# Optimization experiments

Hardware: AMD Instinct MI355X
Metric: run time of the kernel (lower is better)

Reference implementation:

```python
import jax, jax.numpy as jnp
import numpy as np

HIDDEN = 450
DEPTH = 6
ATOM_FDIM = 35          # len(ELEM_LIST)+6+5+1
BOND_FDIM = 5
MAX_NB = 15
N_ATOMS = 20000
N_BONDS = 40000
N_MESS = 16000          # tree messages (row 0 is the zero padding slot)
N_MOLS = 1000


def _linear_init(key, out_dim, in_dim):
    s = 1.0 / np.sqrt(in_dim)
    return jax.random.uniform(key, (out_dim, in_dim), jnp.float32, -s, s)


def setup_inputs() -> dict:
    key = jax.random.key(0)
    ks = jax.random.split(key, 9)
    total_msg = N_MESS + N_BONDS
    fatoms = jax.random.normal(ks[0], (N_ATOMS, ATOM_FDIM), jnp.float32)
    fbonds = jax.random.normal(ks[1], (N_BONDS, ATOM_FDIM + BOND_FDIM), jnp.float32)
    agraph = jax.random.randint(ks[2], (N_ATOMS, MAX_NB), 0, total_msg, jnp.int32)
    bgraph = jax.random.randint(ks[3], (N_BONDS, MAX_NB), 0, total_msg, jnp.int32)
    tree_message = jax.random.normal(ks[4], (N_MESS, HIDDEN), jnp.float32)
    tree_message = tree_message.at[0].set(0.0)  # index 0 = padding message
    # uniform scope: N_MOLS molecules of N_ATOMS//N_MOLS atoms each
    mol_ids = jnp.repeat(jnp.arange(N_MOLS, dtype=jnp.int32), N_ATOMS // N_MOLS)
    W_i = _linear_init(ks[5], HIDDEN, ATOM_FDIM + BOND_FDIM)
    W_h = _linear_init(ks[6], HIDDEN, HIDDEN)
    W_o = _linear_init(ks[7], HIDDEN, ATOM_FDIM + HIDDEN)
    s = 1.0 / np.sqrt(ATOM_FDIM + HIDDEN)
    b_o = jax.random.uniform(ks[8], (HIDDEN,), jnp.float32, -s, s)
    return {"fatoms": fatoms, "fbonds": fbonds, "agraph": agraph, "bgraph": bgraph,
            "mol_ids": mol_ids, "n_mols": N_MOLS, "tree_message": tree_message,
            "W_i": W_i, "W_h": W_h, "W_o": W_o, "b_o": b_o}


def reference(fatoms, fbonds, agraph, bgraph, mol_ids, n_mols, tree_message,
              W_i, W_h, W_o, b_o):
    binput = fbonds @ W_i.T                       # [B, H]
    graph_message = jax.nn.relu(binput)
    for _ in range(DEPTH - 1):                    # static depth loop
        message = jnp.concatenate([tree_message, graph_message], axis=0)  # [M+B, H]
        nei_message = message[bgraph].sum(axis=1)  # gather [B, MAX_NB, H] -> [B, H]
        graph_message = jax.nn.relu(binput + nei_message @ W_h.T)
    message = jnp.concatenate([tree_message, graph_message], axis=0)
    nei_message = message[agraph].sum(axis=1)      # [A, H]
    ainput = jnp.concatenate([fatoms, nei_message], axis=1)  # [A, ATOM_FDIM+H]
    atom_hiddens = jax.nn.relu(ainput @ W_o.T + b_o)          # [A, H]
    # mean over each molecule's atoms (scope)
    sums = jax.ops.segment_sum(atom_hiddens, mol_ids, num_segments=n_mols)
    counts = jax.ops.segment_sum(jnp.ones((atom_hiddens.shape[0], 1), atom_hiddens.dtype),
                                 mol_ids, num_segments=n_mols)
    return sums / counts
```

## Files before the change

kernel.cpp:

```cpp
#include <hip/hip_runtime.h>

#define HIDDEN 450
#define MAX_NB 15
#define N_ATOMS 20000
#define N_BONDS 40000
#define N_MESS  16000
#define N_MOLS  1000
#define KPAD    512
#define MSTRIDE 456

typedef unsigned int uint;
typedef unsigned short ushort;
typedef __bf16 bf16x8 __attribute__((ext_vector_type(8)));
typedef float  f32x4  __attribute__((ext_vector_type(4)));

__device__ __forceinline__ ushort f2bf(float f) {
    uint u = __builtin_bit_cast(uint, f);
    u += 0x7fffu + ((u >> 16) & 1u);
    return (ushort)(u >> 16);
}
__device__ __forceinline__ float bfhi(uint w) {
    return __builtin_bit_cast(float, w & 0xffff0000u);
}
__device__ __forceinline__ float bflo(uint w) {
    return __builtin_bit_cast(float, w << 16);
}

#define GLOADLDS16(g, l) __builtin_amdgcn_global_load_lds( \
    (const __attribute__((address_space(1))) void*)(g),    \
    (__attribute__((address_space(3))) void*)(l), 16, 0, 0)


__global__ __launch_bounds__(256) void pack_tree(const float* __restrict__ tree,
                                                 ushort* __restrict__ tbuf) {
    const int r = blockIdx.x, t = threadIdx.x;
    if (t < 228) {
        uint p = 0;
        if (t < 225) {
            const float2 v = *(const float2*)&tree[(size_t)r * HIDDEN + 2 * t];
            p = (uint)f2bf(v.x) | ((uint)f2bf(v.y) << 16);
        }
        ((uint*)(tbuf + (size_t)r * MSTRIDE))[t] = p;
    }
}

__global__ __launch_bounds__(256) void pack_bonds(const float* __restrict__ fbonds,
                                                  ushort* __restrict__ Abuf) {
    const int r = blockIdx.x * 4 + (threadIdx.x >> 6);
    const int t = threadIdx.x & 63;
    if (r >= N_BONDS) return;
    ushort* row = Abuf + (size_t)r * KPAD;
    if (t < 40) row[t] = f2bf(fbonds[(size_t)r * 40 + t]);
    else        row[t] = 0;
    if (t < 16) row[496 + t] = 0;
}

__global__ __launch_bounds__(256) void pack_atoms(const float* __restrict__ fatoms,
                                                  ushort* __restrict__ Aout) {
    const int r = blockIdx.x * 4 + (threadIdx.x >> 6);
    const int t = threadIdx.x & 63;
    if (r >= N_ATOMS) return;
    ushort* row = Aout + (size_t)r * KPAD;
    if (t < 40) row[t] = (t < 35) ? f2bf(fatoms[(size_t)r * 35 + t]) : (ushort)0;
    if (t < 16) row[496 + t] = 0;
}

__global__ __launch_bounds__(256) void pack_w(const float* __restrict__ W_i,
                                              const float* __restrict__ W_h,
                                              const float* __restrict__ W_o,
                                              ushort* __restrict__ Wcat,
                                              ushort* __restrict__ Wocat) {
    const int n = blockIdx.x;
    for (int c = threadIdx.x; c < KPAD; c += 256) {
        float v = 0.0f, vo = 0.0f;
        if (n < HIDDEN) {
            if (c < 40)       v = W_i[(size_t)n * 40 + c];
            else if (c < 490) v = W_h[(size_t)n * HIDDEN + (c - 40)];
            if (c < 35)       vo = W_o[(size_t)n * 485 + c];
            else if (c >= 40 && c < 490) vo = W_o[(size_t)n * 485 + 35 + (c - 40)];
        }
        Wcat [(size_t)n * KPAD + c] = f2bf(v);
        Wocat[(size_t)n * KPAD + c] = f2bf(vo);
    }
}

__global__ __launch_bounds__(256) void gather_sum(const int* __restrict__ g,
                                                  const ushort* __restrict__ tbuf,
                                                  const ushort* __restrict__ gmsg,
                                                  ushort* __restrict__ dst, int nrows) {
    const int r = blockIdx.x * 4 + (threadIdx.x >> 6);
    const int lane = threadIdx.x & 63;
    if (r >= nrows) return;
    const int* gr = g + (size_t)r * MAX_NB;
    int idx[MAX_NB];
#pragma unroll
    for (int j = 0; j < MAX_NB; ++j) idx[j] = gr[j];
    if (lane >= 57) return;
    const int off = lane * 8;
    float acc[8] = {};
#pragma unroll
    for (int j = 0; j < MAX_NB; ++j) {
        const ushort* row = (idx[j] < N_MESS)
            ? tbuf + (size_t)idx[j] * MSTRIDE
            : gmsg + (size_t)(idx[j] - N_MESS) * MSTRIDE;
        const uint4 w = *(const uint4*)(row + off);
        acc[0] += bflo(w.x); acc[1] += bfhi(w.x);
        acc[2] += bflo(w.y); acc[3] += bfhi(w.y);
        acc[4] += bflo(w.z); acc[5] += bfhi(w.z);
        acc[6] += bflo(w.w); acc[7] += bfhi(w.w);
    }
    uint4 p;
    p.x = (uint)f2bf(acc[0]) | ((uint)f2bf(acc[1]) << 16);
    p.y = (uint)f2bf(acc[2]) | ((uint)f2bf(acc[3]) << 16);
    p.z = (uint)f2bf(acc[4]) | ((uint)f2bf(acc[5]) << 16);
    p.w = (uint)f2bf(acc[6]) | ((uint)f2bf(acc[7]) << 16);
    *(uint4*)(dst + (size_t)r * KPAD + 40 + off) = p;
}

template <int MODE>
__global__ __launch_bounds__(256) void mfma_gemm(const ushort* __restrict__ A, int M,
                                                 const ushort* __restrict__ W, int K,
                                                 const float* __restrict__ bias,
                                                 const int* __restrict__ mol_ids,
                                                 ushort* __restrict__ gout,
                                                 float* __restrict__ aout) {
    __shared__ ushort At[128 * 32];
    __shared__ ushort Wt[128 * 32];
    const int tid  = threadIdx.x;
    const int lane = tid & 63;
    const int wave = tid >> 6;
    const int wm = (wave >> 1) * 64;
    const int wn = (wave & 1) * 64;
    const int m0 = blockIdx.x * 128;
    const int n0 = blockIdx.y * 128;

    const int ob0 = tid * 16;
    const int row0 = ob0 >> 6, ke0 = ((ob0 >> 4) & 3) * 8;
    const int ob1 = ob0 + 4096;
    const int row1 = ob1 >> 6, ke1 = ((ob1 >> 4) & 3) * 8;
    const int ar0 = min(m0 + row0, M - 1);
    const int ar1 = min(m0 + row1, M - 1);

    f32x4 acc[4][4];
#pragma unroll
    for (int i = 0; i < 4; ++i)
#pragma unroll
        for (int j = 0; j < 4; ++j) acc[i][j] = (f32x4){0.f, 0.f, 0.f, 0.f};

#pragma unroll 1
    for (int k0 = 0; k0 < K; k0 += 32) {
        GLOADLDS16(A + (size_t)ar0 * KPAD + k0 + ke0, &At[ob0 >> 1]);
        GLOADLDS16(A + (size_t)ar1 * KPAD + k0 + ke1, &At[ob1 >> 1]);
        GLOADLDS16(W + (size_t)(n0 + row0) * KPAD + k0 + ke0, &Wt[ob0 >> 1]);
        GLOADLDS16(W + (size_t)(n0 + row1) * KPAD + k0 + ke1, &Wt[ob1 >> 1]);
        __syncthreads();

        bf16x8 af[4], wf[4];
#pragma unroll
        for (int t = 0; t < 4; ++t)
            af[t] = *(const bf16x8*)&At[(wm + t * 16 + (lane & 15)) * 32 + (lane >> 4) * 8];
#pragma unroll
        for (int t = 0; t < 4; ++t)
            wf[t] = *(const bf16x8*)&Wt[(wn + t * 16 + (lane & 15)) * 32 + (lane >> 4) * 8];
#pragma unroll
        for (int mt = 0; mt < 4; ++mt)
#pragma unroll
            for (int nt = 0; nt < 4; ++nt)
                acc[mt][nt] = __builtin_amdgcn_mfma_f32_16x16x32_bf16(
                    af[mt], wf[nt], acc[mt][nt], 0, 0, 0);
        __syncthreads();
    }

    const int col_l = lane & 15;
    const int rbase = (lane >> 4) * 4;
#pragma unroll
    for (int mt = 0; mt < 4; ++mt) {
#pragma unroll
        for (int nt = 0; nt < 4; ++nt) {
            const int n = n0 + wn + nt * 16 + col_l;
            if (n >= HIDDEN) continue;
#pragma unroll
            for (int reg = 0; reg < 4; ++reg) {
                const int m = m0 + wm + mt * 16 + rbase + reg;
                if (m >= M) continue;
                float v = acc[mt][nt][reg];
                if (MODE == 0) {
                    v = fmaxf(v, 0.0f);
                    gout[(size_t)m * MSTRIDE + n] = f2bf(v);
                } else {
                    v = fmaxf(v + bias[n], 0.0f);
                    atomicAdd(&aout[(size_t)mol_ids[m] * HIDDEN + n], v);
                }
            }
        }
    }
}

__global__ __launch_bounds__(256) void count_atoms(const int* __restrict__ mol_ids,
                                                   float* __restrict__ counts) {
    const int a = blockIdx.x * 256 + threadIdx.x;
    if (a < N_ATOMS) atomicAdd(&counts[mol_ids[a]], 1.0f);
}
__global__ __launch_bounds__(256) void div_counts(float* __restrict__ out,
                                                  const float* __restrict__ counts) {
    const int i = blockIdx.x * 256 + threadIdx.x;
    if (i < N_MOLS * HIDDEN) out[i] = out[i] / counts[i / HIDDEN];
}

extern "C" void kernel_launch(void* const* d_in, const int* in_sizes, int n_in,
                              void* d_out, int out_size, void* d_ws, size_t ws_size,
                              hipStream_t stream) {
    const float* fatoms  = (const float*)d_in[0];
    const float* fbonds  = (const float*)d_in[1];
    const int*   agraph  = (const int*)d_in[2];
    const int*   bgraph  = (const int*)d_in[3];
    const int*   mol_ids = (const int*)d_in[4];
    const float* tree    = (const float*)d_in[6];
    const float* W_i     = (const float*)d_in[7];
    const float* W_h     = (const float*)d_in[8];
    const float* W_o     = (const float*)d_in[9];
    const float* b_o     = (const float*)d_in[10];
    float* out = (float*)d_out;

    ushort* Abuf  = (ushort*)d_ws;
    ushort* Aout  = Abuf  + (size_t)N_BONDS * KPAD;
    ushort* gmsg  = Aout  + (size_t)N_ATOMS * KPAD;
    ushort* tbuf  = gmsg  + (size_t)N_BONDS * MSTRIDE;
    ushort* Wcat  = tbuf  + (size_t)N_MESS  * MSTRIDE;
    ushort* Wocat = Wcat  + (size_t)KPAD * KPAD;
    float*  counts = (float*)(Wocat + (size_t)KPAD * KPAD);

    (void)hipMemsetAsync(d_out, 0, (size_t)N_MOLS * HIDDEN * sizeof(float), stream);
    (void)hipMemsetAsync(counts, 0, N_MOLS * sizeof(float), stream);
    (void)hipMemsetAsync(gmsg, 0, (size_t)N_BONDS * MSTRIDE * sizeof(ushort), stream);

    const dim3 blk(256);
    pack_tree <<<N_MESS, blk, 0, stream>>>(tree, tbuf);
    pack_bonds<<<(N_BONDS + 3) / 4, blk, 0, stream>>>(fbonds, Abuf);
    pack_atoms<<<(N_ATOMS + 3) / 4, blk, 0, stream>>>(fatoms, Aout);
    pack_w    <<<KPAD, blk, 0, stream>>>(W_i, W_h, W_o, Wcat, Wocat);

    const dim3 gB((N_BONDS + 127) / 128, 4);
    const dim3 gA((N_ATOMS + 127) / 128, 4);

    mfma_gemm<0><<<gB, blk, 0, stream>>>(Abuf, N_BONDS, Wcat, 64,
                                         nullptr, nullptr, gmsg, nullptr);
    for (int it = 0; it < 5; ++it) {
        gather_sum<<<(N_BONDS + 3) / 4, blk, 0, stream>>>(bgraph, tbuf, gmsg,
                                                          Abuf, N_BONDS);
        mfma_gemm<0><<<gB, blk, 0, stream>>>(Abuf, N_BONDS, Wcat, KPAD,
                                             nullptr, nullptr, gmsg, nullptr);
    }
    gather_sum<<<(N_ATOMS + 3) / 4, blk, 0, stream>>>(agraph, tbuf, gmsg,
                                                      Aout, N_ATOMS);
    mfma_gemm<1><<<gA, blk, 0, stream>>>(Aout, N_ATOMS, Wocat, KPAD,
                                         b_o, mol_ids, nullptr, out);

    count_atoms<<<(N_ATOMS + 255) / 256, blk, 0, stream>>>(mol_ids, counts);
    div_counts <<<(N_MOLS * HIDDEN + 255) / 256, blk, 0, stream>>>(out, counts);
}
```

Measured before the change: 970.9 us.

## Register-prefetch GEMM tiles with K=64 padded LDS and reordered grid

The MFMA GEMM now stages A and W tiles through registers instead of direct global-to-LDS loads. The next K=64 chunk is prefetched into registers while the current chunk is computed, and the LDS rows are padded to 72 elements to avoid bank conflicts. The grid is swapped so the four N-tiles of the same M rows run next to each other for better L2 reuse of A, and occupancy is hinted at 3 blocks per CU. The separate memset of the message buffer is dropped because the epilogue now writes zeros into the padding columns, at the cost of more registers and larger LDS per block.

```diff
diff --git a/kernel.cpp b/kernel.cpp
--- a/kernel.cpp
+++ b/kernel.cpp
@@ -8,6 +8,7 @@
 #define N_MOLS  1000
 #define KPAD    512
 #define MSTRIDE 456
+#define LPAD    72
 
 typedef unsigned int uint;
 typedef unsigned short ushort;
@@ -25,10 +26,6 @@
 __device__ __forceinline__ float bflo(uint w) {
     return __builtin_bit_cast(float, w << 16);
 }
-
-#define GLOADLDS16(g, l) __builtin_amdgcn_global_load_lds( \
-    (const __attribute__((address_space(1))) void*)(g),    \
-    (__attribute__((address_space(3))) void*)(l), 16, 0, 0)
 
 
 __global__ __launch_bounds__(256) void pack_tree(const float* __restrict__ tree,
@@ -118,28 +115,26 @@
 }
 
 template <int MODE>
-__global__ __launch_bounds__(256) void mfma_gemm(const ushort* __restrict__ A, int M,
-                                                 const ushort* __restrict__ W, int K,
-                                                 const float* __restrict__ bias,
-                                                 const int* __restrict__ mol_ids,
-                                                 ushort* __restrict__ gout,
-                                                 float* __restrict__ aout) {
-    __shared__ ushort At[128 * 32];
-    __shared__ ushort Wt[128 * 32];
+__global__ __launch_bounds__(256, 3) void mfma_gemm(
+    const ushort* __restrict__ A, int M,
+    const ushort* __restrict__ W, int K,
+    const float* __restrict__ bias, const int* __restrict__ mol_ids,
+    ushort* __restrict__ gout, float* __restrict__ aout) {
+    __shared__ ushort At[128 * LPAD];
+    __shared__ ushort Wt[128 * LPAD];
     const int tid  = threadIdx.x;
     const int lane = tid & 63;
     const int wave = tid >> 6;
     const int wm = (wave >> 1) * 64;
     const int wn = (wave & 1) * 64;
-    const int m0 = blockIdx.x * 128;
-    const int n0 = blockIdx.y * 128;
-
-    const int ob0 = tid * 16;
-    const int row0 = ob0 >> 6, ke0 = ((ob0 >> 4) & 3) * 8;
-    const int ob1 = ob0 + 4096;
-    const int row1 = ob1 >> 6, ke1 = ((ob1 >> 4) & 3) * 8;
-    const int ar0 = min(m0 + row0, M - 1);
-    const int ar1 = min(m0 + row1, M - 1);
+    const int m0 = blockIdx.y * 128;
+    const int n0 = blockIdx.x * 128;
+
+    const int srow = tid >> 1;
+    const int scol = (tid & 1) * 32;
+    const size_t gA = (size_t)min(m0 + srow, M - 1) * KPAD + scol;
+    const size_t gW = (size_t)(n0 + srow) * KPAD + scol;
+    const int lds_off = srow * LPAD + scol;
 
     f32x4 acc[4][4];
 #pragma unroll
@@ -147,28 +142,58 @@
 #pragma unroll
         for (int j = 0; j < 4; ++j) acc[i][j] = (f32x4){0.f, 0.f, 0.f, 0.f};
 
+    uint4 pa[2], pw[2];
+    uint4 pa2[2], pw2[2];
+#pragma unroll
+    for (int c = 0; c < 2; ++c) {
+        pa[c]  = *(const uint4*)&A[gA + c * 8];
+        pa2[c] = *(const uint4*)&A[gA + 16 + c * 8];
+        pw[c]  = *(const uint4*)&W[gW + c * 8];
+        pw2[c] = *(const uint4*)&W[gW + 16 + c * 8];
+    }
+
+    const int lr = lane & 15;
+    const int lk = lane >> 4;
+
 #pragma unroll 1
-    for (int k0 = 0; k0 < K; k0 += 32) {
-        GLOADLDS16(A + (size_t)ar0 * KPAD + k0 + ke0, &At[ob0 >> 1]);
-        GLOADLDS16(A + (size_t)ar1 * KPAD + k0 + ke1, &At[ob1 >> 1]);
-        GLOADLDS16(W + (size_t)(n0 + row0) * KPAD + k0 + ke0, &Wt[ob0 >> 1]);
-        GLOADLDS16(W + (size_t)(n0 + row1) * KPAD + k0 + ke1, &Wt[ob1 >> 1]);
+    for (int k0 = 0; k0 < K; k0 += 64) {
+#pragma unroll
+        for (int c = 0; c < 2; ++c) {
+            *(uint4*)&At[lds_off + c * 8]      = pa[c];
+            *(uint4*)&At[lds_off + 16 + c * 8] = pa2[c];
+            *(uint4*)&Wt[lds_off + c * 8]      = pw[c];
+            *(uint4*)&Wt[lds_off + 16 + c * 8] = pw2[c];
+        }
         __syncthreads();
 
-        bf16x8 af[4], wf[4];
-#pragma unroll
-        for (int t = 0; t < 4; ++t)
-            af[t] = *(const bf16x8*)&At[(wm + t * 16 + (lane & 15)) * 32 + (lane >> 4) * 8];
-#pragma unroll
-        for (int t = 0; t < 4; ++t)
-            wf[t] = *(const bf16x8*)&Wt[(wn + t * 16 + (lane & 15)) * 32 + (lane >> 4) * 8];
-#pragma unroll
-        for (int mt = 0; mt < 4; ++mt)
-#pragma unroll
-            for (int nt = 0; nt < 4; ++nt)
-                acc[mt][nt] = __builtin_amdgcn_mfma_f32_16x16x32_bf16(
-                    af[mt], wf[nt], acc[mt][nt], 0, 0, 0);
-        __syncthreads();
+        if (k0 + 64 < K) {
+            const size_t a = gA + k0 + 64, w = gW + k0 + 64;
+#pragma unroll
+            for (int c = 0; c < 2; ++c) {
+                pa[c]  = *(const uint4*)&A[a + c * 8];
+                pa2[c] = *(const uint4*)&A[a + 16 + c * 8];
+                pw[c]  = *(const uint4*)&W[w + c * 8];
+                pw2[c] = *(const uint4*)&W[w + 16 + c * 8];
+            }
+        }
+
+#pragma unroll
+        for (int h = 0; h < 2; ++h) {
+            bf16x8 af[4], wf[4];
+#pragma unroll
+            for (int s = 0; s < 4; ++s)
+                af[s] = *(const bf16x8*)&At[(wm + s * 16 + lr) * LPAD + h * 32 + lk * 8];
+#pragma unroll
+            for (int s = 0; s < 4; ++s)
+                wf[s] = *(const bf16x8*)&Wt[(wn + s * 16 + lr) * LPAD + h * 32 + lk * 8];
+#pragma unroll
+            for (int mt = 0; mt < 4; ++mt)
+#pragma unroll
+                for (int nt = 0; nt < 4; ++nt)
+                    acc[mt][nt] = __builtin_amdgcn_mfma_f32_16x16x32_bf16(
+                        af[mt], wf[nt], acc[mt][nt], 0, 0, 0);
+        }
+        __builtin_amdgcn_s_barrier();
     }
 
     const int col_l = lane & 15;
@@ -178,18 +203,21 @@
 #pragma unroll
         for (int nt = 0; nt < 4; ++nt) {
             const int n = n0 + wn + nt * 16 + col_l;
-            if (n >= HIDDEN) continue;
 #pragma unroll
             for (int reg = 0; reg < 4; ++reg) {
                 const int m = m0 + wm + mt * 16 + rbase + reg;
                 if (m >= M) continue;
                 float v = acc[mt][nt][reg];
                 if (MODE == 0) {
-                    v = fmaxf(v, 0.0f);
-                    gout[(size_t)m * MSTRIDE + n] = f2bf(v);
+                    if (n < HIDDEN)
+                        gout[(size_t)m * MSTRIDE + n] = f2bf(fmaxf(v, 0.0f));
+                    else if (n < MSTRIDE)
+                        gout[(size_t)m * MSTRIDE + n] = 0;
                 } else {
-                    v = fmaxf(v + bias[n], 0.0f);
-                    atomicAdd(&aout[(size_t)mol_ids[m] * HIDDEN + n], v);
+                    if (n < HIDDEN) {
+                        v = fmaxf(v + bias[n], 0.0f);
+                        atomicAdd(&aout[(size_t)mol_ids[m] * HIDDEN + n], v);
+                    }
                 }
             }
         }
@@ -232,7 +260,6 @@
 
     (void)hipMemsetAsync(d_out, 0, (size_t)N_MOLS * HIDDEN * sizeof(float), stream);
     (void)hipMemsetAsync(counts, 0, N_MOLS * sizeof(float), stream);
-    (void)hipMemsetAsync(gmsg, 0, (size_t)N_BONDS * MSTRIDE * sizeof(ushort), stream);
 
     const dim3 blk(256);
     pack_tree <<<N_MESS, blk, 0, stream>>>(tree, tbuf);
@@ -240,8 +267,8 @@
     pack_atoms<<<(N_ATOMS + 3) / 4, blk, 0, stream>>>(fatoms, Aout);
     pack_w    <<<KPAD, blk, 0, stream>>>(W_i, W_h, W_o, Wcat, Wocat);
 
-    const dim3 gB((N_BONDS + 127) / 128, 4);
-    const dim3 gA((N_ATOMS + 127) / 128, 4);
+    const dim3 gB(4, (N_BONDS + 127) / 128);
+    const dim3 gA(4, (N_ATOMS + 127) / 128);
 
     mfma_gemm<0><<<gB, blk, 0, stream>>>(Abuf, N_BONDS, Wcat, 64,
                                          nullptr, nullptr, gmsg, nullptr);
```

Measured after the change: 1.342 ms. 1.38x slower.
